# Kernel tuning notes

Measured on AMD Instinct MI355X. Metric: run time of the kernel, lower is better.

The kernel has to match this reference:

```python
import jax, jax.numpy as jnp
import numpy as np


def setup_inputs() -> dict:
    key = jax.random.key(0)
    kx, ky = jax.random.split(key)
    x = jax.random.normal(kx, (8, 4096, 3), dtype=jnp.float32)
    y = jax.random.normal(ky, (8, 4096, 3), dtype=jnp.float32)
    return {"x": x, "y": y}


def reference(x, y):
    # Mathematically identical to sum((x[:, :, None] - y[:, None, :])**2, -1)
    # but avoids materializing the [B, n, m, 3] diff tensor.
    x2 = jnp.sum(x * x, axis=-1)              # [B, n]
    y2 = jnp.sum(y * y, axis=-1)              # [B, m]
    xy = jnp.einsum('bnd,bmd->bnm', x, y)     # [B, n, m]
    dist = x2[:, :, None] + y2[:, None, :] - 2.0 * xy  # [B, n, m]
    min_dist_xy = jnp.min(dist, axis=2)       # [B, n] nearest y for each x
    min_dist_yx = jnp.min(dist, axis=1)       # [B, m] nearest x for each y
    return jnp.mean(min_dist_xy, axis=1) + jnp.mean(min_dist_yx, axis=1)  # [B]
```

## Files before the change

kernel.cpp:

```cpp
#include <hip/hip_runtime.h>
#include <math.h>

#define BLK 256
#define NPTS 4096
#define XT 32

using short8 = __attribute__((ext_vector_type(8))) short;
using f32x4  = __attribute__((ext_vector_type(4))) float;

__device__ inline unsigned short f2bf(float f) {
  unsigned u = __float_as_uint(f);
  return (unsigned short)((u + 0x7FFFu + ((u >> 16) & 1u)) >> 16);
}
__device__ inline float bf2f(unsigned short h) {
  return __uint_as_float((unsigned)h << 16);
}
__device__ inline unsigned pk(unsigned short lo, unsigned short hi) {
  return (unsigned)lo | ((unsigned)hi << 16);
}

__global__ __launch_bounds__(BLK, 2) void chamfer_mfma_kernel(
    const float* __restrict__ X, const float* __restrict__ Y,
    float* __restrict__ sums)
{
  __shared__ uint4 rec[4096];

  int bid = blockIdx.x;
  int xt  = bid & 31;
  int b   = (bid >> 5) & 7;
  int dir = bid >> 8;

  const float* xs = (dir ? Y : X) + b * (NPTS * 3);
  const float* ys = (dir ? X : Y) + b * (NPTS * 3);

  int t = threadIdx.x;
  int lane = t & 63;
  int w = t >> 6;
  int g = lane >> 4;
  int c = lane & 15;

  int xbase = xt * 128 + w * 32;
  const float* xpa = xs + (xbase + c) * 3;
  const float* xpb = xs + (xbase + 16 + c) * 3;
  float xa0 = xpa[0], xa1 = xpa[1], xa2 = xpa[2];
  float xb0 = xpb[0], xb1 = xpb[1], xb2 = xpb[2];
  float x2a = fmaf(xa0, xa0, fmaf(xa1, xa1, xa2 * xa2));
  float x2b = fmaf(xb0, xb0, fmaf(xb1, xb1, xb2 * xb2));

  const unsigned short ONE = 0x3F80;
  short8 b0f = (short8)0, b1f = (short8)0;
  {
    unsigned short ha0 = f2bf(xa0), ha1 = f2bf(xa1), ha2 = f2bf(xa2);
    unsigned short la0 = f2bf(xa0 - bf2f(ha0));
    unsigned short la1 = f2bf(xa1 - bf2f(ha1));
    unsigned short la2 = f2bf(xa2 - bf2f(ha2));
    unsigned short hb0 = f2bf(xb0), hb1 = f2bf(xb1), hb2 = f2bf(xb2);
    unsigned short lb0 = f2bf(xb0 - bf2f(hb0));
    unsigned short lb1 = f2bf(xb1 - bf2f(hb1));
    unsigned short lb2 = f2bf(xb2 - bf2f(hb2));
    unsigned short mha0 = f2bf(-2.0f * bf2f(ha0));
    unsigned short mha1 = f2bf(-2.0f * bf2f(ha1));
    unsigned short mha2 = f2bf(-2.0f * bf2f(ha2));
    unsigned short mla0 = f2bf(-2.0f * bf2f(la0));
    unsigned short mla1 = f2bf(-2.0f * bf2f(la1));
    unsigned short mla2 = f2bf(-2.0f * bf2f(la2));
    unsigned short mhb0 = f2bf(-2.0f * bf2f(hb0));
    unsigned short mhb1 = f2bf(-2.0f * bf2f(hb1));
    unsigned short mhb2 = f2bf(-2.0f * bf2f(hb2));
    unsigned short mlb0 = f2bf(-2.0f * bf2f(lb0));
    unsigned short mlb1 = f2bf(-2.0f * bf2f(lb1));
    unsigned short mlb2 = f2bf(-2.0f * bf2f(lb2));
    if (g == 0) {
      b0f[0] = mha0; b0f[1] = mha1; b0f[2] = mha2; b0f[3] = mha0;
      b0f[4] = mha1; b0f[5] = mha2; b0f[6] = mla0; b0f[7] = mla1;
      b1f[0] = mhb0; b1f[1] = mhb1; b1f[2] = mhb2; b1f[3] = mhb0;
      b1f[4] = mhb1; b1f[5] = mhb2; b1f[6] = mlb0; b1f[7] = mlb1;
    } else if (g == 1) {
      b0f[0] = mla2; b0f[1] = mla0; b0f[2] = mla1; b0f[3] = mla2;
      b0f[4] = ONE;  b0f[5] = ONE;  b0f[6] = ONE;  b0f[7] = 0;
      b1f[0] = mlb2; b1f[1] = mlb0; b1f[2] = mlb1; b1f[3] = mlb2;
      b1f[4] = ONE;  b1f[5] = ONE;  b1f[6] = ONE;  b1f[7] = 0;
    }
  }

  float gm0 = __builtin_inff(), gm1 = __builtin_inff();
  f32x4 cz = {0.0f, 0.0f, 0.0f, 0.0f};
  const short8* recp = reinterpret_cast<const short8*>(rec);
  int aoff = (g & 1) * 2048 + c;

  for (int p = 0; p < 2; ++p) {
    #pragma unroll
    for (int i = 0; i < 8; ++i) {
      int yl_ = t + i * 256;
      const float* yp = ys + (p * 2048 + yl_) * 3;
      float y0 = yp[0], y1 = yp[1], y2c = yp[2];
      unsigned short h0 = f2bf(y0), h1 = f2bf(y1), h2 = f2bf(y2c);
      unsigned short l0 = f2bf(y0 - bf2f(h0));
      unsigned short l1 = f2bf(y1 - bf2f(h1));
      unsigned short l2 = f2bf(y2c - bf2f(h2));
      float ysq = fmaf(y0, y0, fmaf(y1, y1, y2c * y2c));
      unsigned short s0 = f2bf(ysq);
      float r1 = ysq - bf2f(s0);
      unsigned short s1 = f2bf(r1);
      unsigned short s2 = f2bf(r1 - bf2f(s1));
      uint4 w0, w1;
      w0.x = pk(h0, h1); w0.y = pk(h2, l0); w0.z = pk(l1, l2); w0.w = pk(h0, h1);
      w1.x = pk(h2, l0); w1.y = pk(l1, l2); w1.z = pk(s0, s1); w1.w = pk(s2, 0);
      rec[yl_] = w0;
      rec[2048 + yl_] = w1;
    }
    __syncthreads();

    #pragma unroll 4
    for (int tile = 0; tile < 128; ++tile) {
      short8 a = recp[aoff + tile * 16];
      f32x4 d0 = __builtin_amdgcn_mfma_f32_16x16x32_bf16(a, b0f, cz, 0, 0, 0);
      f32x4 d1 = __builtin_amdgcn_mfma_f32_16x16x32_bf16(a, b1f, cz, 0, 0, 0);
      float m0 = fminf(fminf(d0[0], d0[1]), d0[2]);
      gm0 = fminf(fminf(m0, d0[3]), gm0);
      float m1 = fminf(fminf(d1[0], d1[1]), d1[2]);
      gm1 = fminf(fminf(m1, d1[3]), gm1);
    }
    __syncthreads();
  }

  gm0 = fminf(gm0, __shfl_xor(gm0, 16, 64));
  gm0 = fminf(gm0, __shfl_xor(gm0, 32, 64));
  gm1 = fminf(gm1, __shfl_xor(gm1, 16, 64));
  gm1 = fminf(gm1, __shfl_xor(gm1, 32, 64));
  float v = (lane < 16) ? (gm0 + x2a) + (gm1 + x2b) : 0.0f;
  #pragma unroll
  for (int mm = 1; mm < 64; mm <<= 1) v += __shfl_xor(v, mm, 64);

  float* red = reinterpret_cast<float*>(rec);
  if (lane == 0) red[w] = v;
  __syncthreads();
  if (t == 0) sums[bid] = (red[0] + red[1]) + (red[2] + red[3]);
}

__global__ __launch_bounds__(512) void chamfer_final_kernel(
    const float* __restrict__ sums, float* __restrict__ out)
{
  __shared__ float gred[16];
  int t = threadIdx.x;
  float v = sums[t];
  #pragma unroll
  for (int mm = 1; mm < 32; mm <<= 1) v += __shfl_xor(v, mm, 64);
  if ((t & 31) == 0) gred[t >> 5] = v;
  __syncthreads();
  if (t < 8) out[t] = (gred[t] + gred[t + 8]) * (1.0f / 4096.0f);
}

__global__ __launch_bounds__(BLK, 2) void chamfer_direct_kernel(
    const float* __restrict__ X, const float* __restrict__ Y,
    float* __restrict__ out)
{
  extern __shared__ float4 shd[];
  int lin = blockIdx.x;
  int xt  = lin & 1;  lin >>= 1;
  int b   = lin & 7;
  int dir = lin >> 3;
  const float* xs = (dir ? Y : X) + b * (NPTS * 3);
  const float* ys = (dir ? X : Y) + b * (NPTS * 3);

  for (int j = threadIdx.x; j < NPTS; j += BLK) {
    float y0 = ys[j * 3 + 0], y1 = ys[j * 3 + 1], y2 = ys[j * 3 + 2];
    shd[j] = make_float4(y0, y1, y2, 0.5f * (y0 * y0 + y1 * y1 + y2 * y2));
  }
  __syncthreads();

  int x0i = xt * (BLK * 8) + threadIdx.x * 8;
  float xf[24];
  const float4* xp = reinterpret_cast<const float4*>(xs + x0i * 3);
  #pragma unroll
  for (int i = 0; i < 6; ++i) {
    float4 p = xp[i];
    xf[i * 4 + 0] = p.x; xf[i * 4 + 1] = p.y;
    xf[i * 4 + 2] = p.z; xf[i * 4 + 3] = p.w;
  }
  float n0[8], n1[8], n2[8], x2h[8], gm[8];
  #pragma unroll
  for (int k = 0; k < 8; ++k) {
    float a = xf[k * 3 + 0], bb = xf[k * 3 + 1], cc = xf[k * 3 + 2];
    n0[k] = -a; n1[k] = -bb; n2[k] = -cc;
    x2h[k] = 0.5f * (a * a + bb * bb + cc * cc);
    gm[k] = __builtin_inff();
  }
  for (int j = 0; j < NPTS; j += 4) {
    float4 p0 = shd[j], p1 = shd[j + 1], p2 = shd[j + 2], p3 = shd[j + 3];
    #pragma unroll
    for (int k = 0; k < 8; ++k) {
      float ga = fmaf(n0[k], p0.x, fmaf(n1[k], p0.y, fmaf(n2[k], p0.z, p0.w)));
      float gb = fmaf(n0[k], p1.x, fmaf(n1[k], p1.y, fmaf(n2[k], p1.z, p1.w)));
      float gc = fmaf(n0[k], p2.x, fmaf(n1[k], p2.y, fmaf(n2[k], p2.z, p2.w)));
      float gd = fmaf(n0[k], p3.x, fmaf(n1[k], p3.y, fmaf(n2[k], p3.z, p3.w)));
      float m  = fminf(fminf(ga, gb), gc);
      gm[k] = fminf(fminf(m, gd), gm[k]);
    }
  }
  float v = 0.0f;
  #pragma unroll
  for (int k = 0; k < 8; ++k) v += 2.0f * (x2h[k] + gm[k]);
  #pragma unroll
  for (int off = 32; off > 0; off >>= 1) v += __shfl_down(v, off, 64);
  __syncthreads();
  float* red = reinterpret_cast<float*>(shd);
  if ((threadIdx.x & 63) == 0) red[threadIdx.x >> 6] = v;
  __syncthreads();
  if (threadIdx.x == 0) {
    float s2 = red[0] + red[1] + red[2] + red[3];
    atomicAdd(&out[b], s2 * (1.0f / 4096.0f));
  }
}

__global__ void zero_out_kernel(float* out)
{
  if (threadIdx.x < 8) out[threadIdx.x] = 0.0f;
}

extern "C" void kernel_launch(void* const* d_in, const int* in_sizes, int n_in,
                              void* d_out, int out_size, void* d_ws, size_t ws_size,
                              hipStream_t stream)
{
  const float* X = (const float*)d_in[0];
  const float* Y = (const float*)d_in[1];
  float* out = (float*)d_out;

  if (ws_size >= (size_t)(2 * 8 * XT) * sizeof(float)) {
    chamfer_mfma_kernel<<<2 * 8 * XT, BLK, 0, stream>>>(X, Y, (float*)d_ws);
    chamfer_final_kernel<<<1, 512, 0, stream>>>((const float*)d_ws, out);
  } else {
    zero_out_kernel<<<1, 64, 0, stream>>>(out);
    chamfer_direct_kernel<<<2 * 8 * 2, BLK, NPTS * sizeof(float4), stream>>>(
        X, Y, out);
  }
}
```

Baseline: 70.88 us.

## Switch to 32x32x16 bf16 MFMA with y-tile split across waves

Replaces the 16x16x32 MFMA inner loop with 32x32x16 MFMA. Each wave now covers all 128 x points of the block in four 32-point groups and a quarter of the y points, instead of owning 32 x points and scanning every y. Per-wave partial minima are merged through shared memory before the sum, which adds a sync and an LDS reduction. The aim is fewer A-fragment LDS loads per MFMA and higher MFMA throughput, at the cost of 16 accumulator registers per result and a longer min reduction.

```diff
diff --git a/kernel.cpp b/kernel.cpp
--- a/kernel.cpp
+++ b/kernel.cpp
@@ -6,7 +6,7 @@
 #define XT 32
 
 using short8 = __attribute__((ext_vector_type(8))) short;
-using f32x4  = __attribute__((ext_vector_type(4))) float;
+using f32x16 = __attribute__((ext_vector_type(16))) float;
 
 __device__ inline unsigned short f2bf(float f) {
   unsigned u = __float_as_uint(f);
@@ -36,57 +36,43 @@
   int t = threadIdx.x;
   int lane = t & 63;
   int w = t >> 6;
-  int g = lane >> 4;
-  int c = lane & 15;
-
-  int xbase = xt * 128 + w * 32;
-  const float* xpa = xs + (xbase + c) * 3;
-  const float* xpb = xs + (xbase + 16 + c) * 3;
-  float xa0 = xpa[0], xa1 = xpa[1], xa2 = xpa[2];
-  float xb0 = xpb[0], xb1 = xpb[1], xb2 = xpb[2];
-  float x2a = fmaf(xa0, xa0, fmaf(xa1, xa1, xa2 * xa2));
-  float x2b = fmaf(xb0, xb0, fmaf(xb1, xb1, xb2 * xb2));
+  int half = lane >> 5;
+  int c = lane & 31;
 
   const unsigned short ONE = 0x3F80;
-  short8 b0f = (short8)0, b1f = (short8)0;
-  {
-    unsigned short ha0 = f2bf(xa0), ha1 = f2bf(xa1), ha2 = f2bf(xa2);
-    unsigned short la0 = f2bf(xa0 - bf2f(ha0));
-    unsigned short la1 = f2bf(xa1 - bf2f(ha1));
-    unsigned short la2 = f2bf(xa2 - bf2f(ha2));
-    unsigned short hb0 = f2bf(xb0), hb1 = f2bf(xb1), hb2 = f2bf(xb2);
-    unsigned short lb0 = f2bf(xb0 - bf2f(hb0));
-    unsigned short lb1 = f2bf(xb1 - bf2f(hb1));
-    unsigned short lb2 = f2bf(xb2 - bf2f(hb2));
-    unsigned short mha0 = f2bf(-2.0f * bf2f(ha0));
-    unsigned short mha1 = f2bf(-2.0f * bf2f(ha1));
-    unsigned short mha2 = f2bf(-2.0f * bf2f(ha2));
-    unsigned short mla0 = f2bf(-2.0f * bf2f(la0));
-    unsigned short mla1 = f2bf(-2.0f * bf2f(la1));
-    unsigned short mla2 = f2bf(-2.0f * bf2f(la2));
-    unsigned short mhb0 = f2bf(-2.0f * bf2f(hb0));
-    unsigned short mhb1 = f2bf(-2.0f * bf2f(hb1));
-    unsigned short mhb2 = f2bf(-2.0f * bf2f(hb2));
-    unsigned short mlb0 = f2bf(-2.0f * bf2f(lb0));
-    unsigned short mlb1 = f2bf(-2.0f * bf2f(lb1));
-    unsigned short mlb2 = f2bf(-2.0f * bf2f(lb2));
-    if (g == 0) {
-      b0f[0] = mha0; b0f[1] = mha1; b0f[2] = mha2; b0f[3] = mha0;
-      b0f[4] = mha1; b0f[5] = mha2; b0f[6] = mla0; b0f[7] = mla1;
-      b1f[0] = mhb0; b1f[1] = mhb1; b1f[2] = mhb2; b1f[3] = mhb0;
-      b1f[4] = mhb1; b1f[5] = mhb2; b1f[6] = mlb0; b1f[7] = mlb1;
-    } else if (g == 1) {
-      b0f[0] = mla2; b0f[1] = mla0; b0f[2] = mla1; b0f[3] = mla2;
-      b0f[4] = ONE;  b0f[5] = ONE;  b0f[6] = ONE;  b0f[7] = 0;
-      b1f[0] = mlb2; b1f[1] = mlb0; b1f[2] = mlb1; b1f[3] = mlb2;
-      b1f[4] = ONE;  b1f[5] = ONE;  b1f[6] = ONE;  b1f[7] = 0;
-    }
-  }
-
-  float gm0 = __builtin_inff(), gm1 = __builtin_inff();
-  f32x4 cz = {0.0f, 0.0f, 0.0f, 0.0f};
+  short8 bf[4];
+  #pragma unroll
+  for (int xg = 0; xg < 4; ++xg) {
+    const float* xp = xs + (xt * 128 + xg * 32 + c) * 3;
+    float x0 = xp[0], x1 = xp[1], x2c = xp[2];
+    unsigned short h0 = f2bf(x0), h1 = f2bf(x1), h2 = f2bf(x2c);
+    unsigned short l0 = f2bf(x0 - bf2f(h0));
+    unsigned short l1 = f2bf(x1 - bf2f(h1));
+    unsigned short l2 = f2bf(x2c - bf2f(h2));
+    unsigned short mh0 = f2bf(-2.0f * bf2f(h0));
+    unsigned short mh1 = f2bf(-2.0f * bf2f(h1));
+    unsigned short mh2 = f2bf(-2.0f * bf2f(h2));
+    unsigned short ml0 = f2bf(-2.0f * bf2f(l0));
+    unsigned short ml1 = f2bf(-2.0f * bf2f(l1));
+    unsigned short ml2 = f2bf(-2.0f * bf2f(l2));
+    short8 v;
+    if (half == 0) {
+      v[0] = mh0; v[1] = mh1; v[2] = mh2; v[3] = mh0;
+      v[4] = mh1; v[5] = mh2; v[6] = ml0; v[7] = ml1;
+    } else {
+      v[0] = ml2; v[1] = ml0; v[2] = ml1; v[3] = ml2;
+      v[4] = ONE; v[5] = ONE; v[6] = ONE; v[7] = 0;
+    }
+    bf[xg] = v;
+  }
+
+  float gm[4];
+  #pragma unroll
+  for (int xg = 0; xg < 4; ++xg) gm[xg] = __builtin_inff();
+  f32x16 cz = {0.0f, 0.0f, 0.0f, 0.0f, 0.0f, 0.0f, 0.0f, 0.0f,
+               0.0f, 0.0f, 0.0f, 0.0f, 0.0f, 0.0f, 0.0f, 0.0f};
   const short8* recp = reinterpret_cast<const short8*>(rec);
-  int aoff = (g & 1) * 2048 + c;
+  int abase = half * 2048 + w * 512 + c;
 
   for (int p = 0; p < 2; ++p) {
     #pragma unroll
@@ -112,30 +98,48 @@
     __syncthreads();
 
     #pragma unroll 4
-    for (int tile = 0; tile < 128; ++tile) {
-      short8 a = recp[aoff + tile * 16];
-      f32x4 d0 = __builtin_amdgcn_mfma_f32_16x16x32_bf16(a, b0f, cz, 0, 0, 0);
-      f32x4 d1 = __builtin_amdgcn_mfma_f32_16x16x32_bf16(a, b1f, cz, 0, 0, 0);
-      float m0 = fminf(fminf(d0[0], d0[1]), d0[2]);
-      gm0 = fminf(fminf(m0, d0[3]), gm0);
-      float m1 = fminf(fminf(d1[0], d1[1]), d1[2]);
-      gm1 = fminf(fminf(m1, d1[3]), gm1);
+    for (int tile = 0; tile < 16; ++tile) {
+      short8 a = recp[abase + tile * 32];
+      #pragma unroll
+      for (int xg = 0; xg < 4; ++xg) {
+        f32x16 d =
+            __builtin_amdgcn_mfma_f32_32x32x16_bf16(a, bf[xg], cz, 0, 0, 0);
+        float m0 = fminf(fminf(d[0], d[1]), d[2]);
+        float m1 = fminf(fminf(d[3], d[4]), d[5]);
+        float m2 = fminf(fminf(d[6], d[7]), d[8]);
+        float m3 = fminf(fminf(d[9], d[10]), d[11]);
+        float m4 = fminf(fminf(d[12], d[13]), d[14]);
+        float n0 = fminf(fminf(m0, m1), m2);
+        float n1 = fminf(fminf(m3, m4), d[15]);
+        gm[xg] = fminf(fminf(n0, n1), gm[xg]);
+      }
     }
     __syncthreads();
   }
 
-  gm0 = fminf(gm0, __shfl_xor(gm0, 16, 64));
-  gm0 = fminf(gm0, __shfl_xor(gm0, 32, 64));
-  gm1 = fminf(gm1, __shfl_xor(gm1, 16, 64));
-  gm1 = fminf(gm1, __shfl_xor(gm1, 32, 64));
-  float v = (lane < 16) ? (gm0 + x2a) + (gm1 + x2b) : 0.0f;
+  #pragma unroll
+  for (int xg = 0; xg < 4; ++xg)
+    gm[xg] = fminf(gm[xg], __shfl_xor(gm[xg], 32, 64));
+
+  float* pf = reinterpret_cast<float*>(rec);
+  if (lane < 32) {
+    #pragma unroll
+    for (int xg = 0; xg < 4; ++xg) pf[w * 128 + xg * 32 + c] = gm[xg];
+  }
+  __syncthreads();
+
+  float v = 0.0f;
+  if (t < 128) {
+    float m = fminf(fminf(pf[t], pf[128 + t]), fminf(pf[256 + t], pf[384 + t]));
+    const float* xp = xs + (xt * 128 + t) * 3;
+    float a0 = xp[0], a1 = xp[1], a2 = xp[2];
+    v = m + fmaf(a0, a0, fmaf(a1, a1, a2 * a2));
+  }
   #pragma unroll
   for (int mm = 1; mm < 64; mm <<= 1) v += __shfl_xor(v, mm, 64);
-
-  float* red = reinterpret_cast<float*>(rec);
-  if (lane == 0) red[w] = v;
-  __syncthreads();
-  if (t == 0) sums[bid] = (red[0] + red[1]) + (red[2] + red[3]);
+  if (lane == 0 && t < 128) pf[512 + w] = v;
+  __syncthreads();
+  if (t == 0) sums[bid] = pf[512] + pf[513];
 }
 
 __global__ __launch_bounds__(512) void chamfer_final_kernel(
```

Result: faster. 68.17 us, median of 2 (-3.8%).
